# Optimization experiments

Measured on AMD Instinct MI355X. Metric: run time of the kernel, lower is better.

Reference implementation:

```python
import jax, jax.numpy as jnp
import numpy as np

STRIDE = (1, 1)
PADDING = ((1, 1), (1, 1))


def setup_inputs() -> dict:
    key = jax.random.key(0)
    k1, k2 = jax.random.split(key)
    x = jax.random.normal(k1, (32, 256, 56, 56), dtype=jnp.float32)
    # kaiming-uniform-like init scale (matches _ConvNd.reset_parameters magnitude roughly)
    fan_in = 256 * 3 * 3
    bound = float(np.sqrt(1.0 / fan_in))
    weight = jax.random.uniform(k2, (256, 256, 3, 3), dtype=jnp.float32,
                                minval=-bound, maxval=bound)
    return {"x": x, "weight": weight}


def reference(x, weight):
    # per-output-filter mean of |w| over (in_ch, kh, kw)
    a = jnp.mean(jnp.abs(weight), axis=(1, 2, 3), keepdims=True)  # [O,1,1,1]
    b = jnp.sign(weight)
    binary_weight = b * a
    out = jax.lax.conv_general_dilated(
        x, binary_weight,
        window_strides=STRIDE,
        padding=PADDING,
        dimension_numbers=("NCHW", "OIHW", "NCHW"),
    )
    return out
```

## Files before the change

kernel.cpp:

```cpp
#include <hip/hip_runtime.h>
#include <cstdint>
#include <cstddef>

#define XP_BYTES 55115776ull
#define WB_OFF   55115776ull
#define AL_OFF   (WB_OFF + 1179648ull)

typedef __bf16 bf16x8 __attribute__((ext_vector_type(8)));
typedef float  f32x4  __attribute__((ext_vector_type(4)));

static __device__ __forceinline__ unsigned short f2bf(float f) {
  union { float f; unsigned int u; } v; v.f = f;
  unsigned int u = v.u;
  u += 0x7FFFu + ((u >> 16) & 1u);
  return (unsigned short)(u >> 16);
}

static __device__ __forceinline__ void async16(void* lds, const void* g) {
  __builtin_amdgcn_global_load_lds(
      (const __attribute__((address_space(1))) unsigned int*)g,
      (__attribute__((address_space(3))) unsigned int*)lds, 16, 0, 0);
}

__global__ void prep_w(const float* __restrict__ w, unsigned short* __restrict__ wb,
                       float* __restrict__ alpha) {
  const int o = blockIdx.x, c = threadIdx.x;
  const float* wr = w + (size_t)(o * 256 + c) * 9;
  float s = 0.f;
#pragma unroll
  for (int tap = 0; tap < 9; ++tap) {
    float v = wr[tap];
    s += fabsf(v);
    unsigned short sg = (v > 0.f) ? 0x3F80u : ((v < 0.f) ? 0xBF80u : 0u);
    wb[(size_t)o * 2304 + tap * 256 + c] = sg;
  }
  __shared__ float red[256];
  red[c] = s;
  __syncthreads();
  for (int d = 128; d > 0; d >>= 1) {
    if (c < d) red[c] += red[c + d];
    __syncthreads();
  }
  if (c == 0) alpha[o] = red[0] * (1.f / 2304.f);
}

__global__ void prep_x(const float* __restrict__ x, unsigned short* __restrict__ xp) {
  const int bx = blockIdx.x;
  const int n = bx / 58, hp = bx % 58;
  const int t = threadIdx.x;
  unsigned short* row = xp + (size_t)(n * 58 + hp) * 58 * 256;

  if (hp == 0 || hp == 57) {
    uint32_t* r32 = (uint32_t*)row;
    for (int i = t; i < 7424; i += 256) r32[i] = 0;
    return;
  }
  const int h = hp - 1;
  const int c2 = (t & 127) * 2;
  const int rep = t >> 7;
  const int w0 = rep * 28;
  const float* x0 = x + ((size_t)(n * 256 + c2) * 56 + h) * 56;
  const float* x1 = x0 + (size_t)56 * 56;

  if (rep == 0) {
    ((uint32_t*)row)[c2 >> 1] = 0;
    ((uint32_t*)(row + 57 * 256))[c2 >> 1] = 0;
  }
#pragma unroll
  for (int i = 0; i < 7; ++i) {
    float4 a = *(const float4*)(x0 + w0 + i * 4);
    float4 b = *(const float4*)(x1 + w0 + i * 4);
    unsigned short va[4] = {f2bf(a.x), f2bf(a.y), f2bf(a.z), f2bf(a.w)};
    unsigned short vb[4] = {f2bf(b.x), f2bf(b.y), f2bf(b.z), f2bf(b.w)};
    const int wbase = w0 + i * 4;
#pragma unroll
    for (int j = 0; j < 4; ++j) {
      uint32_t pack = (uint32_t)va[j] | ((uint32_t)vb[j] << 16);
      ((uint32_t*)(row + (size_t)(wbase + j + 1) * 256))[c2 >> 1] = pack;
    }
  }
}

__global__ __launch_bounds__(256, 3)
void conv_mfma(const unsigned short* __restrict__ xp,
               const unsigned short* __restrict__ wb,
               const float* __restrict__ alpha,
               float* __restrict__ out) {
  __shared__ __align__(16) char lds[16384];
  char* ldsA = lds;
  char* ldsB = lds + 8192;

  const int tid = threadIdx.x;
  const int wave = tid >> 6, lane = tid & 63;
  const int wm = wave >> 1, wn = wave & 1;
  const int o0 = (blockIdx.x & 1) * 128;
  const int pix0 = (blockIdx.x >> 1) * 128;

  const int chunk = lane & 3;
  const int rsub = lane >> 2;

  const char* wbB = (const char*)wb;
  const char* xpB = (const char*)xp;
  const char* gA[2];
  const char* gB[2];
#pragma unroll
  for (int j = 0; j < 2; ++j) {
    const int row = (wave * 2 + j) * 16 + rsub;
    gA[j] = wbB + ((size_t)(o0 + row) * 2304 + chunk * 8) * 2;
    const int pix = pix0 + row;
    const int n = pix / 3136, rem = pix % 3136;
    const int h = rem / 56, w = rem % 56;
    gB[j] = xpB + (size_t)((n * 58 + h) * 58 + w) * 512 + chunk * 16;
  }

  f32x4 acc[4][4];
#pragma unroll
  for (int i = 0; i < 4; ++i)
#pragma unroll
    for (int j = 0; j < 4; ++j) acc[i][j] = (f32x4){0.f, 0.f, 0.f, 0.f};

  const int ar = lane & 15, aq = lane >> 4;

  for (int tap = 0; tap < 9; ++tap) {
    const int kh = tap / 3, kw = tap % 3;
    const int tapoff = (kh * 58 + kw) * 512;
#pragma unroll
    for (int cc = 0; cc < 8; ++cc) {
      const int kA = (tap * 256 + cc * 32) * 2;
      const int kB = tapoff + cc * 64;
      __syncthreads();
      async16(ldsA + (wave * 2 + 0) * 1024, gA[0] + kA);
      async16(ldsA + (wave * 2 + 1) * 1024, gA[1] + kA);
      async16(ldsB + (wave * 2 + 0) * 1024, gB[0] + kB);
      async16(ldsB + (wave * 2 + 1) * 1024, gB[1] + kB);
      __syncthreads();

      bf16x8 af[4], bfr[4];
#pragma unroll
      for (int mi = 0; mi < 4; ++mi)
        af[mi] = *(const bf16x8*)(ldsA + ((wm * 64 + mi * 16 + ar) * 64 + aq * 16));
#pragma unroll
      for (int ni = 0; ni < 4; ++ni)
        bfr[ni] = *(const bf16x8*)(ldsB + ((wn * 64 + ni * 16 + ar) * 64 + aq * 16));
#pragma unroll
      for (int mi = 0; mi < 4; ++mi)
#pragma unroll
        for (int ni = 0; ni < 4; ++ni)
          acc[mi][ni] = __builtin_amdgcn_mfma_f32_16x16x32_bf16(af[mi], bfr[ni], acc[mi][ni], 0, 0, 0);
    }
  }

  int nc[4], rc[4];
#pragma unroll
  for (int ni = 0; ni < 4; ++ni) {
    const int pix = pix0 + wn * 64 + ni * 16 + ar;
    nc[ni] = pix / 3136; rc[ni] = pix % 3136;
  }
#pragma unroll
  for (int mi = 0; mi < 4; ++mi) {
    const int orow = o0 + wm * 64 + mi * 16 + aq * 4;
    float al[4];
#pragma unroll
    for (int r = 0; r < 4; ++r) al[r] = alpha[orow + r];
#pragma unroll
    for (int ni = 0; ni < 4; ++ni) {
      const size_t base = (size_t)nc[ni] * 802816 + (size_t)orow * 3136 + (size_t)rc[ni];
#pragma unroll
      for (int r = 0; r < 4; ++r)
        out[base + (size_t)r * 3136] = acc[mi][ni][r] * al[r];
    }
  }
}

extern "C" void kernel_launch(void* const* d_in, const int* in_sizes, int n_in,
                              void* d_out, int out_size, void* d_ws, size_t ws_size,
                              hipStream_t stream) {
  const float* x = (const float*)d_in[0];
  const float* w = (const float*)d_in[1];
  char* ws = (char*)d_ws;
  unsigned short* xp  = (unsigned short*)ws;
  unsigned short* wbp = (unsigned short*)(ws + WB_OFF);
  float* alpha = (float*)(ws + AL_OFF);
  float* out = (float*)d_out;

  prep_w<<<256, 256, 0, stream>>>(w, wbp, alpha);
  prep_x<<<32 * 58, 256, 0, stream>>>(x, xp);
  conv_mfma<<<1568, 256, 0, stream>>>(xp, wbp, alpha, out);
}
```

Before: 351.5 us.

## Double K-step per barrier, XOR-swizzle LDS, transpose prep_x through shared memory

The conv kernel now loads 64 channels per barrier pair instead of 32, which doubles LDS use to 32KB and halves the number of __syncthreads. An XOR swizzle on 16-byte chunks is added to avoid LDS bank conflicts on fragment reads. Block ordering changes so all pixel tiles for the first output half run before those for the second half, and the occupancy hint goes from 3 to 4. prep_x now transposes NCHW to NHWC through a shared-memory tile, replacing strided uint32 global writes with coalesced ones at the cost of scalar global reads.

```diff
diff --git a/kernel.cpp b/kernel.cpp
--- a/kernel.cpp
+++ b/kernel.cpp
@@ -2,7 +2,6 @@
 #include <cstdint>
 #include <cstddef>
 
-#define XP_BYTES 55115776ull
 #define WB_OFF   55115776ull
 #define AL_OFF   (WB_OFF + 1179648ull)
 
@@ -44,7 +43,8 @@
   if (c == 0) alpha[o] = red[0] * (1.f / 2304.f);
 }
 
-__global__ void prep_x(const float* __restrict__ x, unsigned short* __restrict__ xp) {
+__global__ __launch_bounds__(256) void prep_x(const float* __restrict__ x,
+                                              unsigned short* __restrict__ xp) {
   const int bx = blockIdx.x;
   const int n = bx / 58, hp = bx % 58;
   const int t = threadIdx.x;
@@ -56,61 +56,59 @@
     return;
   }
   const int h = hp - 1;
-  const int c2 = (t & 127) * 2;
-  const int rep = t >> 7;
-  const int w0 = rep * 28;
-  const float* x0 = x + ((size_t)(n * 256 + c2) * 56 + h) * 56;
-  const float* x1 = x0 + (size_t)56 * 56;
+  __shared__ unsigned short tile[56 * 258];
 
-  if (rep == 0) {
-    ((uint32_t*)row)[c2 >> 1] = 0;
-    ((uint32_t*)(row + 57 * 256))[c2 >> 1] = 0;
+  const int w = t & 63, cw = t >> 6;
+  if (w < 56) {
+    const float* src = x + ((size_t)(n * 256 + cw) * 56 + h) * 56 + w;
+#pragma unroll 8
+    for (int k = 0; k < 64; ++k) {
+      tile[w * 258 + (k * 4 + cw)] = f2bf(*src);
+      src += (size_t)4 * 3136;
+    }
   }
+  __syncthreads();
+
+  uint32_t* r32 = (uint32_t*)row;
+  if (t < 128) { r32[t] = 0; r32[57 * 128 + t] = 0; }
 #pragma unroll
-  for (int i = 0; i < 7; ++i) {
-    float4 a = *(const float4*)(x0 + w0 + i * 4);
-    float4 b = *(const float4*)(x1 + w0 + i * 4);
-    unsigned short va[4] = {f2bf(a.x), f2bf(a.y), f2bf(a.z), f2bf(a.w)};
-    unsigned short vb[4] = {f2bf(b.x), f2bf(b.y), f2bf(b.z), f2bf(b.w)};
-    const int wbase = w0 + i * 4;
-#pragma unroll
-    for (int j = 0; j < 4; ++j) {
-      uint32_t pack = (uint32_t)va[j] | ((uint32_t)vb[j] << 16);
-      ((uint32_t*)(row + (size_t)(wbase + j + 1) * 256))[c2 >> 1] = pack;
-    }
+  for (int it = 0; it < 28; ++it) {
+    const int id = it * 256 + t;
+    const int ww = id >> 7, cp = id & 127;
+    const uint32_t lo = tile[ww * 258 + 2 * cp];
+    const uint32_t hi = tile[ww * 258 + 2 * cp + 1];
+    r32[(ww + 1) * 128 + cp] = lo | (hi << 16);
   }
 }
 
-__global__ __launch_bounds__(256, 3)
+__global__ __launch_bounds__(256, 4)
 void conv_mfma(const unsigned short* __restrict__ xp,
                const unsigned short* __restrict__ wb,
                const float* __restrict__ alpha,
                float* __restrict__ out) {
-  __shared__ __align__(16) char lds[16384];
+  __shared__ __align__(16) char lds[32768];
   char* ldsA = lds;
-  char* ldsB = lds + 8192;
+  char* ldsB = lds + 16384;
 
   const int tid = threadIdx.x;
   const int wave = tid >> 6, lane = tid & 63;
   const int wm = wave >> 1, wn = wave & 1;
-  const int o0 = (blockIdx.x & 1) * 128;
-  const int pix0 = (blockIdx.x >> 1) * 128;
+  const int o0 = (blockIdx.x >= 784) ? 128 : 0;
+  const int pix0 = (blockIdx.x % 784) * 128;
 
-  const int chunk = lane & 3;
-  const int rsub = lane >> 2;
+  const int rsub = lane >> 3;
+  const int schunk = (lane & 7) ^ rsub;
 
-  const char* wbB = (const char*)wb;
-  const char* xpB = (const char*)xp;
-  const char* gA[2];
-  const char* gB[2];
+  const char* gA[4];
+  const char* gB[4];
 #pragma unroll
-  for (int j = 0; j < 2; ++j) {
-    const int row = (wave * 2 + j) * 16 + rsub;
-    gA[j] = wbB + ((size_t)(o0 + row) * 2304 + chunk * 8) * 2;
+  for (int j = 0; j < 4; ++j) {
+    const int row = (wave * 4 + j) * 8 + rsub;
+    gA[j] = (const char*)wb + (size_t)(o0 + row) * 4608 + schunk * 16;
     const int pix = pix0 + row;
     const int n = pix / 3136, rem = pix % 3136;
-    const int h = rem / 56, w = rem % 56;
-    gB[j] = xpB + (size_t)((n * 58 + h) * 58 + w) * 512 + chunk * 16;
+    const int h = rem / 56, ww = rem % 56;
+    gB[j] = (const char*)xp + (size_t)((n * 58 + h) * 58 + ww) * 512 + schunk * 16;
   }
 
   f32x4 acc[4][4];
@@ -120,33 +118,39 @@
     for (int j = 0; j < 4; ++j) acc[i][j] = (f32x4){0.f, 0.f, 0.f, 0.f};
 
   const int ar = lane & 15, aq = lane >> 4;
+  const int sw = ar & 7;
 
   for (int tap = 0; tap < 9; ++tap) {
-    const int kh = tap / 3, kw = tap % 3;
-    const int tapoff = (kh * 58 + kw) * 512;
+    const int tapoff = ((tap / 3) * 58 + (tap % 3)) * 512;
 #pragma unroll
-    for (int cc = 0; cc < 8; ++cc) {
-      const int kA = (tap * 256 + cc * 32) * 2;
-      const int kB = tapoff + cc * 64;
+    for (int cc = 0; cc < 4; ++cc) {
+      const int kA = tap * 512 + cc * 128;
+      const int kB = tapoff + cc * 128;
       __syncthreads();
-      async16(ldsA + (wave * 2 + 0) * 1024, gA[0] + kA);
-      async16(ldsA + (wave * 2 + 1) * 1024, gA[1] + kA);
-      async16(ldsB + (wave * 2 + 0) * 1024, gB[0] + kB);
-      async16(ldsB + (wave * 2 + 1) * 1024, gB[1] + kB);
+#pragma unroll
+      for (int j = 0; j < 4; ++j) {
+        async16(ldsA + (wave * 4 + j) * 1024, gA[j] + kA);
+        async16(ldsB + (wave * 4 + j) * 1024, gB[j] + kB);
+      }
       __syncthreads();
-
-      bf16x8 af[4], bfr[4];
 #pragma unroll
-      for (int mi = 0; mi < 4; ++mi)
-        af[mi] = *(const bf16x8*)(ldsA + ((wm * 64 + mi * 16 + ar) * 64 + aq * 16));
+      for (int kk = 0; kk < 2; ++kk) {
+        bf16x8 af[4], bfr[4];
 #pragma unroll
-      for (int ni = 0; ni < 4; ++ni)
-        bfr[ni] = *(const bf16x8*)(ldsB + ((wn * 64 + ni * 16 + ar) * 64 + aq * 16));
-#pragma unroll
-      for (int mi = 0; mi < 4; ++mi)
+        for (int mi = 0; mi < 4; ++mi)
+          af[mi] = *(const bf16x8*)(ldsA + (wm * 64 + mi * 16 + ar) * 128 +
+                                    (((kk * 4 + aq) ^ sw) * 16));
 #pragma unroll
         for (int ni = 0; ni < 4; ++ni)
-          acc[mi][ni] = __builtin_amdgcn_mfma_f32_16x16x32_bf16(af[mi], bfr[ni], acc[mi][ni], 0, 0, 0);
+          bfr[ni] = *(const bf16x8*)(ldsB + (wn * 64 + ni * 16 + ar) * 128 +
+                                     (((kk * 4 + aq) ^ sw) * 16));
+#pragma unroll
+        for (int mi = 0; mi < 4; ++mi)
+#pragma unroll
+          for (int ni = 0; ni < 4; ++ni)
+            acc[mi][ni] = __builtin_amdgcn_mfma_f32_16x16x32_bf16(af[mi], bfr[ni],
+                                                                  acc[mi][ni], 0, 0, 0);
+      }
     }
   }
 
```

Result: no change. 357.1 us (+1.6%).
